# Optimization experiments

Measured on AMD Instinct MI355X. Metric: run time of the kernel, lower is better.

## Reference

```python
import jax, jax.numpy as jnp
import numpy as np

QLEN, MLEN, D, H = 1024, 1024, 1024, 16
DH = D // H
KLEN = QLEN + MLEN
SCALE = 1.0 / np.sqrt(DH).astype(np.float32)
W_STD = 0.02


def setup_inputs() -> dict:
    key = jax.random.key(0)
    ks = jax.random.split(key, 14)
    inputs = jax.random.normal(ks[0], (QLEN, 1, D), jnp.float32)
    r = jax.random.normal(ks[1], (KLEN, D), jnp.float32)
    u = jax.random.normal(ks[2], (H, DH), jnp.float32) * W_STD
    v = jax.random.normal(ks[3], (H, DH), jnp.float32) * W_STD
    mem = jax.random.normal(ks[4], (MLEN, 1, D), jnp.float32)
    # causal mask over concatenated [mem, inputs] keys: True = masked
    attn_mask = jnp.triu(jnp.ones((QLEN, KLEN), bool), k=MLEN + 1)
    W_qkv = jax.random.normal(ks[5], (3 * D, D), jnp.float32) * W_STD
    W_r = jax.random.normal(ks[6], (D, D), jnp.float32) * W_STD
    W_o = jax.random.normal(ks[7], (D, D), jnp.float32) * W_STD
    W_ih = jax.random.normal(ks[8], (3 * D, D), jnp.float32) * W_STD
    W_hh = jax.random.normal(ks[9], (3 * D, D), jnp.float32) * W_STD
    b_ih = jnp.zeros((3 * D,), jnp.float32)
    b_hh = jnp.zeros((3 * D,), jnp.float32)
    h0 = jnp.zeros((1, 1, D), jnp.float32)  # GRU hidden, forces batch=1
    return {"inputs": inputs, "r": r, "u": u, "v": v, "attn_mask": attn_mask,
            "mem": mem, "W_qkv": W_qkv, "W_r": W_r, "W_o": W_o,
            "W_ih": W_ih, "W_hh": W_hh, "b_ih": b_ih, "b_hh": b_hh, "h0": h0}


def _rel_shift(x):
    # Transformer-XL relative shift; x: [qlen, klen, b, n]
    q, k, b, n = x.shape
    zp = jnp.zeros((q, 1, b, n), x.dtype)
    xp = jnp.concatenate([zp, x], axis=1)          # [q, k+1, b, n]
    xp = xp.reshape(k + 1, q, b, n)[1:]            # drop first row
    return xp.reshape(q, k, b, n)


def reference(inputs, r, u, v, attn_mask, mem, W_qkv, W_r, W_o,
              W_ih, W_hh, b_ih, b_hh, h0):
    qlen, b, d = inputs.shape
    cat = jnp.concatenate([mem, inputs], axis=0)        # [klen, b, d]
    klen = cat.shape[0]
    w_heads = cat @ W_qkv.T                             # [klen, b, 3d]
    q_h, k_h, v_h = jnp.split(w_heads, 3, axis=-1)
    q_h = q_h[-qlen:].reshape(qlen, b, H, DH)
    k_h = k_h.reshape(klen, b, H, DH)
    v_h = v_h.reshape(klen, b, H, DH)
    r_k = (r @ W_r.T).reshape(klen, H, DH)              # relative key heads

    AC = jnp.einsum('ibnd,jbnd->ijbn', q_h + u, k_h)    # content score
    BD = _rel_shift(jnp.einsum('ibnd,jnd->ijbn', q_h + v, r_k))  # position score
    score = (AC + BD) * SCALE                           # [q, k, b, n]
    score = jnp.where(attn_mask[:, :, None, None], jnp.float32(-1e30), score)
    probs = jax.nn.softmax(score, axis=1)

    attn_vec = jnp.einsum('ijbn,jbnd->ibnd', probs, v_h).reshape(qlen, b, d)
    y = attn_vec @ W_o.T                                # [q, b, d]

    # 1-layer GRU over time (PyTorch gate order r, z, n)
    x_proj = y @ W_ih.T + b_ih                          # [q, b, 3d]

    def step(h, xt):
        gh = h @ W_hh.T + b_hh
        xr, xz, xn = jnp.split(xt, 3, axis=-1)
        hr, hz, hn = jnp.split(gh, 3, axis=-1)
        rg = jax.nn.sigmoid(xr + hr)
        zg = jax.nn.sigmoid(xz + hz)
        ng = jnp.tanh(xn + rg * hn)
        h_new = (1.0 - zg) * ng + zg * h
        return h_new, h_new

    _, ys = jax.lax.scan(step, h0[0], x_proj)           # h0[0]: [b, d]
    return ys, probs
```

## Files before the change

### kernel.cpp

```cpp
#include <hip/hip_runtime.h>
#include <hip/hip_bf16.h>
#include <math.h>

#define QL   1024
#define ML   1024
#define KL   2048
#define DM   1024
#define NH   16
#define DH   64
#define SCL  0.125f
#define GRU_BLOCKS 128
#define GRU_ELPB   8

static __device__ __forceinline__ float dot4(const float4& a, const float4& b) {
    return a.x*b.x + a.y*b.y + a.z*b.z + a.w*b.w;
}

__global__ __launch_bounds__(256) void gemm_nt(
    const float* __restrict__ A, const float* __restrict__ B,
    const float* __restrict__ bias, float* __restrict__ C,
    int M, int N, int K, int skipM, int skipN)
{
    const int bx = blockIdx.x, by = blockIdx.y;
    if (by < skipM && bx < skipN) return;
    __shared__ float As[2][8][128];
    __shared__ float Bs[2][8][128];
    const int tid  = threadIdx.x;
    const int trow = tid >> 1;
    const int tcol = (tid & 1) << 2;
    const float* Ap = A + (size_t)(by*128 + trow)*K + tcol;
    const float* Bp = B + (size_t)(bx*128 + trow)*K + tcol;
    const int tx = tid & 15, ty = tid >> 4;
    float acc[8][8] = {};

    {
        float4 a4 = *(const float4*)(Ap);
        float4 b4 = *(const float4*)(Bp);
        As[0][tcol+0][trow] = a4.x; As[0][tcol+1][trow] = a4.y;
        As[0][tcol+2][trow] = a4.z; As[0][tcol+3][trow] = a4.w;
        Bs[0][tcol+0][trow] = b4.x; Bs[0][tcol+1][trow] = b4.y;
        Bs[0][tcol+2][trow] = b4.z; Bs[0][tcol+3][trow] = b4.w;
    }
    __syncthreads();

    int buf = 0;
    for (int k0 = 8; k0 <= K; k0 += 8) {
        float4 an, bn;
        const bool more = (k0 < K);
        if (more) {
            an = *(const float4*)(Ap + k0);
            bn = *(const float4*)(Bp + k0);
        }
        #pragma unroll
        for (int kk = 0; kk < 8; kk++) {
            float4 a0 = *(const float4*)&As[buf][kk][ty*8];
            float4 a1 = *(const float4*)&As[buf][kk][ty*8+4];
            float4 b0 = *(const float4*)&Bs[buf][kk][tx*8];
            float4 b1 = *(const float4*)&Bs[buf][kk][tx*8+4];
            const float ar[8] = {a0.x,a0.y,a0.z,a0.w,a1.x,a1.y,a1.z,a1.w};
            const float br[8] = {b0.x,b0.y,b0.z,b0.w,b1.x,b1.y,b1.z,b1.w};
            #pragma unroll
            for (int r = 0; r < 8; r++)
                #pragma unroll
                for (int c = 0; c < 8; c++)
                    acc[r][c] += ar[r]*br[c];
        }
        if (more) {
            const int nb = buf ^ 1;
            As[nb][tcol+0][trow] = an.x; As[nb][tcol+1][trow] = an.y;
            As[nb][tcol+2][trow] = an.z; As[nb][tcol+3][trow] = an.w;
            Bs[nb][tcol+0][trow] = bn.x; Bs[nb][tcol+1][trow] = bn.y;
            Bs[nb][tcol+2][trow] = bn.z; Bs[nb][tcol+3][trow] = bn.w;
            __syncthreads();
            buf = nb;
        }
    }

    const int m0 = by*128 + ty*8;
    const int n0 = bx*128 + tx*8;
    float bb[8] = {0,0,0,0,0,0,0,0};
    if (bias) {
        float4 q0 = *(const float4*)(bias + n0);
        float4 q1 = *(const float4*)(bias + n0 + 4);
        bb[0]=q0.x; bb[1]=q0.y; bb[2]=q0.z; bb[3]=q0.w;
        bb[4]=q1.x; bb[5]=q1.y; bb[6]=q1.z; bb[7]=q1.w;
    }
    #pragma unroll
    for (int r = 0; r < 8; r++) {
        float4 o0, o1;
        o0.x = acc[r][0]+bb[0]; o0.y = acc[r][1]+bb[1];
        o0.z = acc[r][2]+bb[2]; o0.w = acc[r][3]+bb[3];
        o1.x = acc[r][4]+bb[4]; o1.y = acc[r][5]+bb[5];
        o1.z = acc[r][6]+bb[6]; o1.w = acc[r][7]+bb[7];
        *(float4*)&C[(size_t)(m0+r)*N + n0]     = o0;
        *(float4*)&C[(size_t)(m0+r)*N + n0 + 4] = o1;
    }
}

__global__ __launch_bounds__(256) void wd_kernel(
    const float* __restrict__ rk, const float* __restrict__ u_,
    const float* __restrict__ v_, float* __restrict__ wd)
{
    int idx = blockIdx.x*256 + threadIdx.x;
    if (idx >= NH*KL) return;
    int n = idx >> 11, jr = idx & (KL-1);
    const float* rp = rk + (size_t)jr*DM + n*DH;
    const float* up = u_ + n*DH;
    const float* vp = v_ + n*DH;
    float s = 0.f;
    #pragma unroll
    for (int d4 = 0; d4 < 16; d4++) {
        float4 r4 = *(const float4*)(rp + d4*4);
        float4 uu = *(const float4*)(up + d4*4);
        float4 vv = *(const float4*)(vp + d4*4);
        s += (vv.x-uu.x)*r4.x + (vv.y-uu.y)*r4.y + (vv.z-uu.z)*r4.z + (vv.w-uu.w)*r4.w;
    }
    wd[idx] = s;
}

__global__ __launch_bounds__(256) void score_kernel(
    const float* __restrict__ wh, const float* __restrict__ rk,
    const float* __restrict__ u_, const float* __restrict__ wd,
    float* __restrict__ sc)
{
    const int jt = blockIdx.x, it = blockIdx.y, n = blockIdx.z;
    const int i0 = it*64, j0 = jt*64;
    if (j0 > i0 + 1087) return;
    __shared__ float squ[64*64];
    __shared__ float sk [64*64];
    __shared__ float sr [128*64];
    __shared__ float swd[128];
    const int tid = threadIdx.x;
    #pragma unroll
    for (int rr = 0; rr < 4; rr++) {
        int p = tid + 256*rr;
        int row = p >> 4, c4 = p & 15;
        int phys = (c4 ^ ((row >> 2) & 15)) << 2;
        float4 q4 = *(const float4*)&wh[(size_t)(ML + i0 + row)*3072 + n*DH + (c4<<2)];
        float4 u4 = *(const float4*)&u_[n*DH + (c4<<2)];
        float4 t4; t4.x=q4.x+u4.x; t4.y=q4.y+u4.y; t4.z=q4.z+u4.z; t4.w=q4.w+u4.w;
        *(float4*)&squ[row*64 + phys] = t4;
        float4 k4 = *(const float4*)&wh[(size_t)(j0 + row)*3072 + DM + n*DH + (c4<<2)];
        *(float4*)&sk[row*64 + phys] = k4;
    }
    const int jr0 = j0 - i0 + 960;
    #pragma unroll
    for (int rr = 0; rr < 8; rr++) {
        int p = tid + 256*rr;
        int row = p >> 4, c4 = p & 15;
        int phys = (c4 ^ ((row >> 2) & 15)) << 2;
        int jr = jr0 + row;
        float4 r4;
        if (jr >= 0 && jr < KL) r4 = *(const float4*)&rk[(size_t)jr*DM + n*DH + (c4<<2)];
        else { r4.x = r4.y = r4.z = r4.w = 0.f; }
        *(float4*)&sr[row*64 + phys] = r4;
    }
    if (tid < 128) {
        int jr = jr0 + tid;
        swd[tid] = (jr >= 0 && jr < KL) ? wd[n*KL + jr] : 0.f;
    }
    __syncthreads();

    const int tj2 = tid & 15, ti2 = tid >> 4;
    const int rbase = tj2*4 - ti2*4 + 60;
    float acc[4][4] = {};
    #pragma unroll
    for (int dc = 0; dc < 16; dc++) {
        float4 qa[4], kb[4], rv[7];
        #pragma unroll
        for (int a = 0; a < 4; a++) {
            int row = ti2*4 + a;
            qa[a] = *(const float4*)&squ[row*64 + ((dc ^ ((row>>2)&15)) << 2)];
        }
        #pragma unroll
        for (int b_ = 0; b_ < 4; b_++) {
            int row = tj2*4 + b_;
            kb[b_] = *(const float4*)&sk[row*64 + ((dc ^ ((row>>2)&15)) << 2)];
        }
        #pragma unroll
        for (int o = 0; o < 7; o++) {
            int row = rbase + o;
            rv[o] = *(const float4*)&sr[row*64 + ((dc ^ ((row>>2)&15)) << 2)];
        }
        #pragma unroll
        for (int a = 0; a < 4; a++)
            #pragma unroll
            for (int b_ = 0; b_ < 4; b_++)
                acc[a][b_] += dot4(qa[a], kb[b_]) + dot4(qa[a], rv[3 + b_ - a]);
    }
    #pragma unroll
    for (int a = 0; a < 4; a++) {
        int i = i0 + ti2*4 + a;
        float4 o;
        o.x = (acc[a][0] + swd[rbase + 3 + 0 - a]) * SCL;
        o.y = (acc[a][1] + swd[rbase + 3 + 1 - a]) * SCL;
        o.z = (acc[a][2] + swd[rbase + 3 + 2 - a]) * SCL;
        o.w = (acc[a][3] + swd[rbase + 3 + 3 - a]) * SCL;
        *(float4*)&sc[((size_t)i*NH + n)*KL + j0 + (tj2<<2)] = o;
    }
}

__global__ __launch_bounds__(512) void softmaxT_kernel(float* __restrict__ sc)
{
    const int i = blockIdx.x;
    const int tid = threadIdx.x;
    __shared__ float ld[16*2052];
    __shared__ float sinv[16];
    float* slab = sc + (size_t)i*KL*NH;
    #pragma unroll
    for (int rr = 0; rr < 16; rr++) {
        int p = tid + 512*rr;
        int nn = p >> 9, j = (p & 511) << 2;
        float4 f = *(const float4*)(slab + ((size_t)nn << 11) + j);
        *(float4*)&ld[nn*2052 + j] = f;
    }
    __syncthreads();
    const int g = tid >> 5, tl = tid & 31;
    const int jmax = i + ML;
    float m = -3.4e38f;
    for (int k = 0; k < 64; k++) {
        int j = tl + (k << 5);
        if (j <= jmax) m = fmaxf(m, ld[g*2052 + j]);
    }
    #pragma unroll
    for (int off = 1; off <= 16; off <<= 1) m = fmaxf(m, __shfl_xor(m, off, 64));
    float ssum = 0.f;
    for (int k = 0; k < 64; k++) {
        int j = tl + (k << 5);
        float e = 0.f;
        if (j <= jmax) { e = __expf(ld[g*2052 + j] - m); ssum += e; }
        ld[g*2052 + j] = e;
    }
    #pragma unroll
    for (int off = 1; off <= 16; off <<= 1) ssum += __shfl_xor(ssum, off, 64);
    if (tl == 0) sinv[g] = 1.f / ssum;
    __syncthreads();
    #pragma unroll
    for (int rr = 0; rr < 16; rr++) {
        int p = tid + 512*rr;
        int j = p >> 2, n0 = (p & 3) << 2;
        float4 o;
        o.x = ld[(n0+0)*2052 + j] * sinv[n0+0];
        o.y = ld[(n0+1)*2052 + j] * sinv[n0+1];
        o.z = ld[(n0+2)*2052 + j] * sinv[n0+2];
        o.w = ld[(n0+3)*2052 + j] * sinv[n0+3];
        *(float4*)(slab + (size_t)p*4) = o;
    }
}

__global__ __launch_bounds__(512) void pv_kernel(
    const float* __restrict__ sc, const float* __restrict__ wh,
    float* __restrict__ attn)
{
    const int it = blockIdx.x >> 1, dh = blockIdx.x & 1;
    const int i0 = it*8;
    const int tid = threadIdx.x;
    __shared__ float Ps[8*16*20];
    __shared__ float Vs[16][512];
    const int col = dh*512 + tid;
    const int nn = col >> 6;
    float acc[8] = {};
    const int jlast = i0 + 7 + ML;
    const int nch = (jlast + 16) >> 4;
    for (int ch = 0; ch < nch; ch++) {
        const int j0 = ch << 4;
        __syncthreads();
        {
            int ii = tid >> 6, rem = tid & 63, jj = rem >> 2, n0 = (rem & 3) << 2;
            float4 f = *(const float4*)(sc + ((size_t)(i0+ii)*KL + j0 + jj)*NH + n0);
            Ps[(ii*16 + n0+0)*20 + jj] = f.x;
            Ps[(ii*16 + n0+1)*20 + jj] = f.y;
            Ps[(ii*16 + n0+2)*20 + jj] = f.z;
            Ps[(ii*16 + n0+3)*20 + jj] = f.w;
        }
        #pragma unroll
        for (int rr = 0; rr < 4; rr++) {
            int p = tid + 512*rr;
            int row = p >> 7, c4 = (p & 127) << 2;
            float4 f = *(const float4*)&wh[(size_t)(j0+row)*3072 + 2048 + dh*512 + c4];
            *(float4*)&Vs[row][c4] = f;
        }
        __syncthreads();
        #pragma unroll
        for (int jq = 0; jq < 4; jq++) {
            float4 pv[8];
            #pragma unroll
            for (int ii = 0; ii < 8; ii++)
                pv[ii] = *(const float4*)&Ps[(ii*16 + nn)*20 + jq*4];
            #pragma unroll
            for (int jj = 0; jj < 4; jj++) {
                float vv = Vs[jq*4 + jj][tid];
                #pragma unroll
                for (int ii = 0; ii < 8; ii++)
                    acc[ii] += ((const float*)&pv[ii])[jj] * vv;
            }
        }
    }
    #pragma unroll
    for (int ii = 0; ii < 8; ii++)
        attn[(size_t)(i0+ii)*DM + col] = acc[ii];
}

__global__ __launch_bounds__(512) void gru_persistent(
    const float* __restrict__ xp,
    const float* __restrict__ Whh,
    const float* __restrict__ bhh,
    const float* __restrict__ h0,
    float* __restrict__ ys,
    unsigned long long* __restrict__ hpack)
{
    __shared__ float wlds[3][GRU_ELPB][DM];
    __shared__ float hlds[DM];
    const int b = blockIdx.x;
    const int tid = threadIdx.x;
    const int w = tid >> 6, l = tid & 63;
    const int dg = b*GRU_ELPB + w;

    #pragma unroll
    for (int k = 0; k < 12; k++) {
        int idx = tid + 512*k;
        int g   = idx >> 11;
        int rem = idx & 2047;
        int e   = rem >> 8;
        int c   = rem & 255;
        float4 f = *(const float4*)&Whh[(size_t)(g*DM + b*GRU_ELPB + e)*DM + (c<<2)];
        *(float4*)&wlds[g][e][c<<2] = f;
    }
    float bh0=0.f, bh1=0.f, bh2=0.f, hreg=0.f;
    if (l == 0) {
        bh0 = bhh[dg]; bh1 = bhh[dg + DM]; bh2 = bhh[dg + 2*DM];
        hreg = h0[dg];
    }

    bool bail = false;
    for (int t = 0; t < QL; t++) {
        float xr=0.f, xz=0.f, xn=0.f;
        if (l == 0) {
            const float* xrow = xp + (size_t)t*3072 + dg;
            xr = xrow[0]; xz = xrow[DM]; xn = xrow[2*DM];
        }
        if (t == 0) {
            hlds[tid]       = h0[tid];
            hlds[tid + 512] = h0[tid + 512];
        } else if (!bail) {
            const unsigned long long* hp = hpack + ((size_t)(t & 1) << 10);
            #define GRU_LDA(i) __hip_atomic_load(&hp[tid + (i)*512], \
                __ATOMIC_RELAXED, __HIP_MEMORY_SCOPE_AGENT)
            unsigned long long a0 = GRU_LDA(0), b0 = GRU_LDA(1);
            unsigned long long a1 = GRU_LDA(0), b1 = GRU_LDA(1);
            unsigned long long a2 = GRU_LDA(0), b2 = GRU_LDA(1);
            unsigned long long v0, v1;
            int guard = 0;
            for (;;) {
                if ((unsigned)(a0 >> 32) >= (unsigned)t &&
                    (unsigned)(b0 >> 32) >= (unsigned)t) { v0 = a0; v1 = b0; break; }
                a0 = a1; b0 = b1;
                a1 = a2; b1 = b2;
                a2 = GRU_LDA(0); b2 = GRU_LDA(1);
                if (++guard > (1<<18)) { bail = true; v0 = GRU_LDA(0); v1 = GRU_LDA(1); break; }
            }
            #undef GRU_LDA
            hlds[tid]       = __uint_as_float((unsigned)v0);
            hlds[tid + 512] = __uint_as_float((unsigned)v1);
        }
        __syncthreads();

        float s0=0.f, s1=0.f, s2=0.f;
        #pragma unroll
        for (int c = 0; c < 4; c++) {
            const int base = c*256 + l*4;
            float4 h4 = *(const float4*)&hlds[base];
            float4 w0 = *(const float4*)&wlds[0][w][base];
            float4 w1 = *(const float4*)&wlds[1][w][base];
            float4 w2 = *(const float4*)&wlds[2][w][base];
            s0 += dot4(w0, h4);
            s1 += dot4(w1, h4);
            s2 += dot4(w2, h4);
        }
        #pragma unroll
        for (int off = 32; off >= 1; off >>= 1) {
            s0 += __shfl_xor(s0, off, 64);
            s1 += __shfl_xor(s1, off, 64);
            s2 += __shfl_xor(s2, off, 64);
        }
        if (l == 0) {
            const float hr = s0 + bh0;
            const float hz = s1 + bh1;
            const float hn = s2 + bh2;
            const float rg = 1.f/(1.f + __expf(-(xr + hr)));
            const float zg = 1.f/(1.f + __expf(-(xz + hz)));
            const float e2 = __expf(2.f*(xn + rg*hn));
            const float ng = (e2 - 1.f) / (e2 + 1.f);
            const float hnew = (1.f - zg)*ng + zg*hreg;
            hreg = hnew;
            unsigned long long pk = (unsigned long long)__float_as_uint(hnew)
                                  | ((unsigned long long)(unsigned)(t+1) << 32);
            __hip_atomic_store(&hpack[(((size_t)(t+1) & 1) << 10) + dg], pk,
                               __ATOMIC_RELAXED, __HIP_MEMORY_SCOPE_AGENT);
            ys[(size_t)t*DM + dg] = hnew;
        }
    }
}

extern "C" void kernel_launch(void* const* d_in, const int* in_sizes, int n_in,
                              void* d_out, int out_size, void* d_ws, size_t ws_size,
                              hipStream_t stream) {
    const float* inputs = (const float*)d_in[0];
    const float* r_in   = (const float*)d_in[1];
    const float* u_in   = (const float*)d_in[2];
    const float* v_in   = (const float*)d_in[3];
    const float* mem    = (const float*)d_in[5];
    const float* Wqkv   = (const float*)d_in[6];
    const float* Wr     = (const float*)d_in[7];
    const float* Wo     = (const float*)d_in[8];
    const float* Wih    = (const float*)d_in[9];
    const float* Whh    = (const float*)d_in[10];
    const float* b_ih   = (const float*)d_in[11];
    const float* b_hh   = (const float*)d_in[12];
    const float* h0     = (const float*)d_in[13];

    float* out = (float*)d_out;
    float* ys  = out;
    float* sc  = out + (size_t)QL*DM;

    float* ws      = (float*)d_ws;
    float* cat     = ws;
    float* wheads  = cat    + (size_t)KL*DM;
    float* rk      = wheads + (size_t)KL*3072;
    float* wd      = rk     + (size_t)KL*DM;
    float* attn    = wd     + (size_t)NH*KL;
    float* ybuf    = attn   + (size_t)QL*DM;
    float* xproj   = ybuf   + (size_t)QL*DM;
    unsigned long long* hpack = (unsigned long long*)(xproj + (size_t)QL*3072);

    hipMemcpyAsync(cat,            mem,    (size_t)ML*DM*4, hipMemcpyDeviceToDevice, stream);
    hipMemcpyAsync(cat + (size_t)ML*DM, inputs, (size_t)QL*DM*4, hipMemcpyDeviceToDevice, stream);
    hipMemsetAsync(hpack, 0, 2*DM*sizeof(unsigned long long), stream);

    gemm_nt<<<dim3(24,16), 256, 0, stream>>>(cat, Wqkv, nullptr, wheads, KL, 3072, DM, 8, 8);
    gemm_nt<<<dim3(8,16), 256, 0, stream>>>(r_in, Wr, nullptr, rk, KL, DM, DM, 0, 0);
    wd_kernel<<<128, 256, 0, stream>>>(rk, u_in, v_in, wd);
    score_kernel<<<dim3(32,16,16), 256, 0, stream>>>(wheads, rk, u_in, wd, sc);
    softmaxT_kernel<<<QL, 512, 0, stream>>>(sc);
    pv_kernel<<<256, 512, 0, stream>>>(sc, wheads, attn);
    gemm_nt<<<dim3(8,8), 256, 0, stream>>>(attn, Wo, nullptr, ybuf, QL, DM, DM, 0, 0);
    gemm_nt<<<dim3(24,8), 256, 0, stream>>>(ybuf, Wih, b_ih, xproj, QL, 3072, DM, 0, 0);
    gru_persistent<<<GRU_BLOCKS, 512, 0, stream>>>(xproj, Whh, b_hh, h0, ys, hpack);
}
```

Baseline: 3.306 ms.

## Replace FP32 SIMT GEMMs with split-bf16 three-pass MFMA GEMM

Rewrites the shared GEMM kernel to use bf16 MFMA matrix instructions. Each fp32 operand is split into high and low bf16 parts, and three MFMA passes (hh, hl, lh) approximate fp32 accuracy. The goal is to move the four projection GEMMs off scalar FMA onto the matrix cores, at the cost of extra conversion work and some lost precision from the dropped lo*lo term. The epilogue now writes scalar, strided stores instead of float4.

Result: faster. 2.892 ms (-12.5%).

```diff
diff --git a/kernel.cpp b/kernel.cpp
--- a/kernel.cpp
+++ b/kernel.cpp
@@ -12,88 +12,115 @@
 #define GRU_BLOCKS 128
 #define GRU_ELPB   8
 
+typedef __attribute__((ext_vector_type(8))) short bfrag;
+typedef __attribute__((ext_vector_type(4))) float facc;
+
 static __device__ __forceinline__ float dot4(const float4& a, const float4& b) {
     return a.x*b.x + a.y*b.y + a.z*b.z + a.w*b.w;
 }
 
-__global__ __launch_bounds__(256) void gemm_nt(
+static __device__ __forceinline__ unsigned bf16_rne(float x) {
+    unsigned u = __float_as_uint(x);
+    return (u + 0x7FFF + ((u >> 16) & 1)) >> 16;
+}
+static __device__ __forceinline__ void bfsplit(float a, short& h, short& l) {
+    unsigned uh = bf16_rne(a);
+    h = (short)uh;
+    float ah = __uint_as_float(uh << 16);
+    l = (short)bf16_rne(a - ah);
+}
+
+__global__ __launch_bounds__(256) void gemm_nt_mfma(
     const float* __restrict__ A, const float* __restrict__ B,
     const float* __restrict__ bias, float* __restrict__ C,
     int M, int N, int K, int skipM, int skipN)
 {
     const int bx = blockIdx.x, by = blockIdx.y;
     if (by < skipM && bx < skipN) return;
-    __shared__ float As[2][8][128];
-    __shared__ float Bs[2][8][128];
-    const int tid  = threadIdx.x;
-    const int trow = tid >> 1;
-    const int tcol = (tid & 1) << 2;
-    const float* Ap = A + (size_t)(by*128 + trow)*K + tcol;
-    const float* Bp = B + (size_t)(bx*128 + trow)*K + tcol;
-    const int tx = tid & 15, ty = tid >> 4;
-    float acc[8][8] = {};
-
-    {
-        float4 a4 = *(const float4*)(Ap);
-        float4 b4 = *(const float4*)(Bp);
-        As[0][tcol+0][trow] = a4.x; As[0][tcol+1][trow] = a4.y;
-        As[0][tcol+2][trow] = a4.z; As[0][tcol+3][trow] = a4.w;
-        Bs[0][tcol+0][trow] = b4.x; Bs[0][tcol+1][trow] = b4.y;
-        Bs[0][tcol+2][trow] = b4.z; Bs[0][tcol+3][trow] = b4.w;
-    }
-    __syncthreads();
-
-    int buf = 0;
-    for (int k0 = 8; k0 <= K; k0 += 8) {
-        float4 an, bn;
-        const bool more = (k0 < K);
-        if (more) {
-            an = *(const float4*)(Ap + k0);
-            bn = *(const float4*)(Bp + k0);
-        }
-        #pragma unroll
-        for (int kk = 0; kk < 8; kk++) {
-            float4 a0 = *(const float4*)&As[buf][kk][ty*8];
-            float4 a1 = *(const float4*)&As[buf][kk][ty*8+4];
-            float4 b0 = *(const float4*)&Bs[buf][kk][tx*8];
-            float4 b1 = *(const float4*)&Bs[buf][kk][tx*8+4];
-            const float ar[8] = {a0.x,a0.y,a0.z,a0.w,a1.x,a1.y,a1.z,a1.w};
-            const float br[8] = {b0.x,b0.y,b0.z,b0.w,b1.x,b1.y,b1.z,b1.w};
-            #pragma unroll
-            for (int r = 0; r < 8; r++)
-                #pragma unroll
-                for (int c = 0; c < 8; c++)
-                    acc[r][c] += ar[r]*br[c];
-        }
-        if (more) {
-            const int nb = buf ^ 1;
-            As[nb][tcol+0][trow] = an.x; As[nb][tcol+1][trow] = an.y;
-            As[nb][tcol+2][trow] = an.z; As[nb][tcol+3][trow] = an.w;
-            Bs[nb][tcol+0][trow] = bn.x; Bs[nb][tcol+1][trow] = bn.y;
-            Bs[nb][tcol+2][trow] = bn.z; Bs[nb][tcol+3][trow] = bn.w;
-            __syncthreads();
-            buf = nb;
-        }
-    }
-
-    const int m0 = by*128 + ty*8;
-    const int n0 = bx*128 + tx*8;
-    float bb[8] = {0,0,0,0,0,0,0,0};
-    if (bias) {
-        float4 q0 = *(const float4*)(bias + n0);
-        float4 q1 = *(const float4*)(bias + n0 + 4);
-        bb[0]=q0.x; bb[1]=q0.y; bb[2]=q0.z; bb[3]=q0.w;
-        bb[4]=q1.x; bb[5]=q1.y; bb[6]=q1.z; bb[7]=q1.w;
-    }
-    #pragma unroll
-    for (int r = 0; r < 8; r++) {
-        float4 o0, o1;
-        o0.x = acc[r][0]+bb[0]; o0.y = acc[r][1]+bb[1];
-        o0.z = acc[r][2]+bb[2]; o0.w = acc[r][3]+bb[3];
-        o1.x = acc[r][4]+bb[4]; o1.y = acc[r][5]+bb[5];
-        o1.z = acc[r][6]+bb[6]; o1.w = acc[r][7]+bb[7];
-        *(float4*)&C[(size_t)(m0+r)*N + n0]     = o0;
-        *(float4*)&C[(size_t)(m0+r)*N + n0 + 4] = o1;
+    __shared__ short Ah[128*40], Al[128*40], Bh[128*40], Bl[128*40];
+    const int tid = threadIdx.x;
+    const int wv = tid >> 6, ln = tid & 63;
+    const int wr = wv >> 1, wc = wv & 1;
+    const int lm = ln & 15, lk = ln >> 4;
+    facc acc[4][4] = {};
+
+    const int srow = tid >> 1;
+    const int scol = (tid & 1) << 4;
+    const float* Ap = A + (size_t)(by*128 + srow)*K + scol;
+    const float* Bp = B + (size_t)(bx*128 + srow)*K + scol;
+
+    float4 ar[4], br[4];
+    #pragma unroll
+    for (int c = 0; c < 4; c++) {
+        ar[c] = *(const float4*)(Ap + c*4);
+        br[c] = *(const float4*)(Bp + c*4);
+    }
+
+    for (int k0 = 0; k0 < K; k0 += 32) {
+        bfrag a_h0, a_h1, a_l0, a_l1, b_h0, b_h1, b_l0, b_l1;
+        #pragma unroll
+        for (int c = 0; c < 4; c++) {
+            const float av[4] = {ar[c].x, ar[c].y, ar[c].z, ar[c].w};
+            const float bv[4] = {br[c].x, br[c].y, br[c].z, br[c].w};
+            #pragma unroll
+            for (int q = 0; q < 4; q++) {
+                const int e = c*4 + q;
+                short h, l;
+                bfsplit(av[q], h, l);
+                if (e < 8) { a_h0[e] = h; a_l0[e] = l; }
+                else       { a_h1[e-8] = h; a_l1[e-8] = l; }
+                bfsplit(bv[q], h, l);
+                if (e < 8) { b_h0[e] = h; b_l0[e] = l; }
+                else       { b_h1[e-8] = h; b_l1[e-8] = l; }
+            }
+        }
+        __syncthreads();
+        *(bfrag*)&Ah[srow*40 + scol    ] = a_h0;
+        *(bfrag*)&Ah[srow*40 + scol + 8] = a_h1;
+        *(bfrag*)&Al[srow*40 + scol    ] = a_l0;
+        *(bfrag*)&Al[srow*40 + scol + 8] = a_l1;
+        *(bfrag*)&Bh[srow*40 + scol    ] = b_h0;
+        *(bfrag*)&Bh[srow*40 + scol + 8] = b_h1;
+        *(bfrag*)&Bl[srow*40 + scol    ] = b_l0;
+        *(bfrag*)&Bl[srow*40 + scol + 8] = b_l1;
+        __syncthreads();
+        if (k0 + 32 < K) {
+            #pragma unroll
+            for (int c = 0; c < 4; c++) {
+                ar[c] = *(const float4*)(Ap + k0 + 32 + c*4);
+                br[c] = *(const float4*)(Bp + k0 + 32 + c*4);
+            }
+        }
+        bfrag fah[4], fal[4], fbh[4], fbl[4];
+        #pragma unroll
+        for (int i = 0; i < 4; i++) {
+            const int rA = wr*64 + i*16 + lm;
+            fah[i] = *(const bfrag*)&Ah[rA*40 + lk*8];
+            fal[i] = *(const bfrag*)&Al[rA*40 + lk*8];
+            const int rB = wc*64 + i*16 + lm;
+            fbh[i] = *(const bfrag*)&Bh[rB*40 + lk*8];
+            fbl[i] = *(const bfrag*)&Bl[rB*40 + lk*8];
+        }
+        #pragma unroll
+        for (int i = 0; i < 4; i++)
+            #pragma unroll
+            for (int j = 0; j < 4; j++) {
+                acc[i][j] = __builtin_amdgcn_mfma_f32_16x16x32_bf16(fah[i], fbh[j], acc[i][j], 0, 0, 0);
+                acc[i][j] = __builtin_amdgcn_mfma_f32_16x16x32_bf16(fah[i], fbl[j], acc[i][j], 0, 0, 0);
+                acc[i][j] = __builtin_amdgcn_mfma_f32_16x16x32_bf16(fal[i], fbh[j], acc[i][j], 0, 0, 0);
+            }
+    }
+
+    const int m0 = by*128 + wr*64 + lk*4;
+    const int n0 = bx*128 + wc*64 + lm;
+    #pragma unroll
+    for (int j = 0; j < 4; j++) {
+        const float bj = bias ? bias[n0 + j*16] : 0.f;
+        #pragma unroll
+        for (int i = 0; i < 4; i++)
+            #pragma unroll
+            for (int r = 0; r < 4; r++)
+                C[(size_t)(m0 + i*16 + r)*N + n0 + j*16] = acc[i][j][r] + bj;
     }
 }
 
@@ -437,13 +464,13 @@
     hipMemcpyAsync(cat + (size_t)ML*DM, inputs, (size_t)QL*DM*4, hipMemcpyDeviceToDevice, stream);
     hipMemsetAsync(hpack, 0, 2*DM*sizeof(unsigned long long), stream);
 
-    gemm_nt<<<dim3(24,16), 256, 0, stream>>>(cat, Wqkv, nullptr, wheads, KL, 3072, DM, 8, 8);
-    gemm_nt<<<dim3(8,16), 256, 0, stream>>>(r_in, Wr, nullptr, rk, KL, DM, DM, 0, 0);
+    gemm_nt_mfma<<<dim3(24,16), 256, 0, stream>>>(cat, Wqkv, nullptr, wheads, KL, 3072, DM, 8, 8);
+    gemm_nt_mfma<<<dim3(8,16), 256, 0, stream>>>(r_in, Wr, nullptr, rk, KL, DM, DM, 0, 0);
     wd_kernel<<<128, 256, 0, stream>>>(rk, u_in, v_in, wd);
     score_kernel<<<dim3(32,16,16), 256, 0, stream>>>(wheads, rk, u_in, wd, sc);
     softmaxT_kernel<<<QL, 512, 0, stream>>>(sc);
     pv_kernel<<<256, 512, 0, stream>>>(sc, wheads, attn);
-    gemm_nt<<<dim3(8,8), 256, 0, stream>>>(attn, Wo, nullptr, ybuf, QL, DM, DM, 0, 0);
-    gemm_nt<<<dim3(24,8), 256, 0, stream>>>(ybuf, Wih, b_ih, xproj, QL, 3072, DM, 0, 0);
+    gemm_nt_mfma<<<dim3(8,8), 256, 0, stream>>>(attn, Wo, nullptr, ybuf, QL, DM, DM, 0, 0);
+    gemm_nt_mfma<<<dim3(24,8), 256, 0, stream>>>(ybuf, Wih, b_ih, xproj, QL, 3072, DM, 0, 0);
     gru_persistent<<<GRU_BLOCKS, 512, 0, stream>>>(xproj, Whh, b_hh, h0, ys, hpack);
 }
```
